# Optimization experiments

Measured on AMD Instinct MI355X. Metric: run time of the kernel, lower is better.

## Reference

```python
import jax, jax.numpy as jnp
import numpy as np

B, T, F, U, M = 4096, 16, 256, 512, 8
DELTA_T = 0.04

# ln_tau_table: tau = 1, 10^0.5, 10^1.0, ... -> ln(tau) = i * 0.5*ln(10)
LN_TAU = (jnp.arange(M, dtype=jnp.float32) * (0.5 * np.log(10.0))).astype(jnp.float32)
DECAY = jnp.exp(-DELTA_T / (LN_TAU + 1e-7))  # [M]


def setup_inputs() -> dict:
    key = jax.random.key(0)
    ks = jax.random.split(key, 9)
    s = lambda fan_in: 1.0 / np.sqrt(fan_in)
    return {
        "x": jax.random.normal(ks[0], (B, T, F), dtype=jnp.float32),
        "W_r": jax.random.normal(ks[1], (F + U, U * M), dtype=jnp.float32) * s(F + U),
        "b_r": jax.random.normal(ks[2], (U * M,), dtype=jnp.float32) * 0.01,
        "W_q": jax.random.normal(ks[3], (F + U, U), dtype=jnp.float32) * s(F + U),
        "b_q": jax.random.normal(ks[4], (U,), dtype=jnp.float32) * 0.01,
        "W_s": jax.random.normal(ks[5], (F + U, U * M), dtype=jnp.float32) * s(F + U),
        "b_s": jax.random.normal(ks[6], (U * M,), dtype=jnp.float32) * 0.01,
        "W_out": jax.random.normal(ks[7], (U, 3), dtype=jnp.float32) * s(U),
        "b_out": jax.random.normal(ks[8], (3,), dtype=jnp.float32) * 0.01,
    }


def _ctgru_forward(x, W_r, b_r, W_q, b_q, W_s, b_s, W_out, b_out):
    def step(h_hat, x_t):  # h_hat: [B,U,M], x_t: [B,F]
        h = h_hat.sum(axis=2)                              # [B,U]
        fused = jnp.concatenate([x_t, h], axis=1)          # [B,F+U]
        ln_tau_r = (fused @ W_r + b_r).reshape(-1, U, M)   # [B,U,M]
        r_ki = jax.nn.softmax(-jnp.square(ln_tau_r - LN_TAU), axis=2)
        q_in = jnp.concatenate([x_t, jnp.sum(r_ki * h_hat, axis=2)], axis=1)
        q_k = jnp.tanh(q_in @ W_q + b_q)[:, :, None]       # [B,U,1]
        ln_tau_s = (fused @ W_s + b_s).reshape(-1, U, M)
        s_ki = jax.nn.softmax(-jnp.square(ln_tau_s - LN_TAU), axis=2)
        h_next = ((1.0 - s_ki) * h_hat + s_ki * q_k) * DECAY
        return h_next, h_next.sum(axis=2)                  # carry, hidden [B,U]

    h0 = jnp.zeros((x.shape[0], U, M), dtype=x.dtype)
    _, hiddens = jax.lax.scan(step, h0, jnp.swapaxes(x, 0, 1))  # hiddens: [T,B,U]
    outputs = jnp.swapaxes(hiddens, 0, 1)                  # [B,T,U]
    return outputs @ W_out + b_out                         # [B,T,3]


def reference(x, W_r, b_r, W_q, b_q, W_s, b_s, W_out, b_out):
    return _ctgru_forward(x, W_r, b_r, W_q, b_q, W_s, b_s, W_out, b_out)
```

## Files before the change

kernel.cpp:

```cpp
#include <hip/hip_runtime.h>
#include <hip/hip_bf16.h>
#include <math.h>

#define B_   4096
#define T_   16
#define F_   256
#define U_   512
#define M_   8
#define K_   768
#define NRS  4096
#define NC   8192
#define LNT  1.1512925f

typedef __bf16 bf16_t;
typedef bf16_t bf16x8 __attribute__((ext_vector_type(8)));
typedef bf16_t bf16x4 __attribute__((ext_vector_type(4)));
typedef float  f32x4  __attribute__((ext_vector_type(4)));

__device__ inline void gl_lds16(const void* g, void* lds) {
    __builtin_amdgcn_global_load_lds(
        (const __attribute__((address_space(1))) unsigned int*)g,
        (__attribute__((address_space(3))) unsigned int*)lds, 16, 0, 0);
}

#define VMCNT(n) asm volatile("s_waitcnt vmcnt(" #n ")" ::: "memory")
#define LGKM0()  asm volatile("s_waitcnt lgkmcnt(0)" ::: "memory")
#define BAR()    __builtin_amdgcn_s_barrier()

__device__ inline void stageA(bf16_t* dst, const bf16_t* xt, const bf16_t* hp,
                              int m0, int k0, int tid) {
    const int r = tid >> 2;
    const int c = ((tid & 3) ^ ((tid >> 3) & 3)) * 8;
    const bf16_t *s0, *s1;
    if (k0 < F_) {
        s0 = xt + (size_t)(m0 + r) * F_ + k0 + c;
        s1 = xt + (size_t)(m0 + r + 128) * F_ + k0 + c;
    } else {
        s0 = hp + (size_t)(m0 + r) * U_ + (k0 - F_) + c;
        s1 = hp + (size_t)(m0 + r + 128) * U_ + (k0 - F_) + c;
    }
    gl_lds16(s0, (char*)dst + tid * 16);
    gl_lds16(s1, (char*)dst + (tid + 512) * 16);
}

__device__ inline void stageB(bf16_t* dst, const bf16_t* Bt, int n0, int k0, int tid) {
    const int r = tid >> 2;
    const int c = ((tid & 3) ^ ((tid >> 3) & 3)) * 8;
    gl_lds16(Bt + (size_t)(n0 + r) * K_ + k0 + c,       (char*)dst + tid * 16);
    gl_lds16(Bt + (size_t)(n0 + r + 128) * K_ + k0 + c, (char*)dst + (tid + 512) * 16);
}

__device__ inline void ds_read4(const bf16_t* base, bf16x8 (&v)[4]) {
    v[0] = *(const bf16x8*)(base);
    v[1] = *(const bf16x8*)(base + 512);
    v[2] = *(const bf16x8*)(base + 1024);
    v[3] = *(const bf16x8*)(base + 1536);
}

template <int H>
__device__ inline void mfma16(f32x4 (&acc)[8][4], const bf16x8 (&a)[4],
                              const bf16x8 (&b)[4]) {
    __builtin_amdgcn_s_setprio(1);
#pragma unroll
    for (int i = 0; i < 4; ++i)
#pragma unroll
        for (int j = 0; j < 4; ++j)
            acc[H * 4 + i][j] = __builtin_amdgcn_mfma_f32_16x16x32_bf16(
                a[i], b[j], acc[H * 4 + i][j], 0, 0, 0);
    __builtin_amdgcn_s_setprio(0);
}

__global__ __launch_bounds__(512, 2) void gemm_rs_p2(
    const bf16_t* __restrict__ xt,
    const bf16_t* __restrict__ hprev,
    const bf16_t* __restrict__ Bt,
    const float*  __restrict__ biasP,
    const bf16_t* __restrict__ hhat,
    bf16_t* __restrict__ rh,
    bf16_t* __restrict__ sbuf)
{
    __shared__ bf16_t Asl[2][256 * 32];
    __shared__ bf16_t Bsl[2][256 * 32];

    const int tid  = threadIdx.x;
    const int lane = tid & 63;
    const int wave = tid >> 6;

    const int lin = blockIdx.y * 16 + blockIdx.x;
    const int xcd = lin & 7, q = lin >> 3;
    const int m0 = ((xcd >> 1) * 4 + (q & 3)) * 256;
    const int n0 = ((xcd & 1) * 16 + (q >> 2)) * 256;

    const int wm = wave >> 2;
    const int wn = wave & 3;
    const int lr = lane & 15;
    const int kq = lane >> 4;
    const int cr = (kq ^ ((lr >> 1) & 3)) * 8;

    const int aoff0 = (wm * 128 + lr) * 32 + cr;
    const int aoff1 = (wm * 128 + 64 + lr) * 32 + cr;
    const int boff  = (wn * 64 + lr) * 32 + cr;

    f32x4 acc[8][4] = {};
    bf16x8 a[4], b[4];

    stageA(&Asl[0][0], xt, hprev, m0, 0, tid);
    stageB(&Bsl[0][0], Bt, n0, 0, tid);
    VMCNT(0);
    BAR();

#define TILE(T, SFLAG)                                                        \
  {                                                                           \
    const int p_ = (T) & 1, pn_ = p_ ^ 1;                                     \
    if (SFLAG) {                                                              \
      stageA(&Asl[pn_][0], xt, hprev, m0, ((T) + 1) * 32, tid);               \
      stageB(&Bsl[pn_][0], Bt, n0, ((T) + 1) * 32, tid);                      \
    }                                                                         \
    ds_read4(&Asl[p_][0] + aoff0, a);                                         \
    ds_read4(&Bsl[p_][0] + boff, b);                                          \
    LGKM0();                                                                  \
    mfma16<0>(acc, a, b);                                                     \
    ds_read4(&Asl[p_][0] + aoff1, a);                                         \
    LGKM0();                                                                  \
    mfma16<1>(acc, a, b);                                                     \
    VMCNT(0);                                                                 \
    BAR();                                                                    \
  }

    for (int tt = 0; tt < 22; tt += 2) { TILE(tt, 1); TILE(tt + 1, 1); }
    TILE(22, 1);
    TILE(23, 0);
#undef TILE

    const int nb  = n0 + wn * 64;
    const int u3  = lane & 7;
    const int m0v = ((lane >> 3) & 1) * 4;
    const bool is_r = nb < NRS;

    float bj[4];
#pragma unroll
    for (int j = 0; j < 4; ++j) bj[j] = biasP[nb + j * 16 + lr];

#pragma unroll
    for (int mi = 0; mi < 8; ++mi) {
        const int rowb = m0 + wm * 128 + mi * 16 + kq * 4;
#pragma unroll
        for (int r = 0; r < 4; ++r) {
            const int row = rowb + r;
            float e[4], sum = 0.f;
#pragma unroll
            for (int j = 0; j < 4; ++j) {
                float v = acc[mi][j][r] + bj[j];
                float d = v - (float)(m0v + j) * LNT;
                e[j] = __expf(-d * d);
                sum += e[j];
            }
            sum += __shfl_xor(sum, 8, 64);
            const float inv = 1.0f / sum;
            if (is_r) {
                bf16x4 h4 = *(const bf16x4*)(hhat + (size_t)row * NRS + nb + u3 * 8 + m0v);
                float rhv = 0.f;
#pragma unroll
                for (int j = 0; j < 4; ++j) rhv += e[j] * inv * (float)h4[j];
                rhv += __shfl_xor(rhv, 8, 64);
                if ((lane & 8) == 0)
                    rh[(size_t)row * U_ + (nb >> 3) + u3] = (bf16_t)rhv;
            } else {
                bf16x4 pv;
#pragma unroll
                for (int j = 0; j < 4; ++j) pv[j] = (bf16_t)(e[j] * inv);
                *(bf16x4*)(sbuf + (size_t)row * NRS + (nb - NRS) + u3 * 8 + m0v) = pv;
            }
        }
    }
}

__global__ __launch_bounds__(256) void gemm_q_up(
    const bf16_t* __restrict__ xt,
    const bf16_t* __restrict__ rh,
    const bf16_t* __restrict__ Bq,
    const float*  __restrict__ bq,
    const bf16_t* __restrict__ sbuf,
    bf16_t* __restrict__ hhat,
    bf16_t* __restrict__ hnext)
{
    __shared__ bf16_t Al[2][64 * 32];
    __shared__ bf16_t Bl[2][64 * 32];

    const int tid  = threadIdx.x;
    const int lane = tid & 63;
    const int wave = tid >> 6;
    const int m0 = blockIdx.x * 64;
    const int n0 = blockIdx.y * 64;
    const int wm = (wave & 1) * 32;
    const int wn = (wave >> 1) * 32;
    const int lr = lane & 15;
    const int kq = lane >> 4;

    f32x4 acc[2][2] = {};

    const int rA = tid >> 2;
    const int kc = (tid & 3) * 8;

    for (int kk = 0; kk < K_; kk += 64) {
        const bf16_t* arow;
        int cbase;
        if (kk < F_) { arow = xt + (size_t)(m0 + rA) * F_; cbase = kk; }
        else         { arow = rh + (size_t)(m0 + rA) * U_; cbase = kk - F_; }

        __syncthreads();
        gl_lds16(arow + cbase + kc,      (char*)&Al[0][0] + tid * 16);
        gl_lds16(arow + cbase + 32 + kc, (char*)&Al[1][0] + tid * 16);
        gl_lds16(Bq + (size_t)(n0 + rA) * K_ + kk + kc,      (char*)&Bl[0][0] + tid * 16);
        gl_lds16(Bq + (size_t)(n0 + rA) * K_ + kk + 32 + kc, (char*)&Bl[1][0] + tid * 16);
        __syncthreads();

#pragma unroll
        for (int s = 0; s < 2; s++) {
            bf16x8 af[2], bfr[2];
#pragma unroll
            for (int i = 0; i < 2; i++)
                af[i] = *(const bf16x8*)(&Al[s][0] + (wm + i * 16 + lr) * 32 + kq * 8);
#pragma unroll
            for (int i = 0; i < 2; i++)
                bfr[i] = *(const bf16x8*)(&Bl[s][0] + (wn + i * 16 + lr) * 32 + kq * 8);
#pragma unroll
            for (int i = 0; i < 2; i++)
#pragma unroll
                for (int j = 0; j < 2; j++)
                    acc[i][j] = __builtin_amdgcn_mfma_f32_16x16x32_bf16(
                        af[i], bfr[j], acc[i][j], 0, 0, 0);
        }
    }

    const float DEC[8] = {0.0f, 0.9658531f, 0.9827783f, 0.9884856f,
                          0.9913518f, 0.9930754f, 0.9942261f, 0.9950489f};

#pragma unroll
    for (int i = 0; i < 2; i++) {
        const int rowb = m0 + wm + i * 16 + kq * 4;
#pragma unroll
        for (int j = 0; j < 2; j++) {
            const int u = n0 + wn + j * 16 + lr;
            const float bv = bq[u];
#pragma unroll
            for (int r = 0; r < 4; r++) {
                const int row = rowb + r;
                const float q = tanhf(acc[i][j][r] + bv);
                const size_t base = (size_t)row * NRS + u * 8;
                bf16x8 s8 = *(const bf16x8*)(sbuf + base);
                bf16x8 h8 = *(const bf16x8*)(hhat + base);
                bf16x8 ho;
                float hs = 0.f;
#pragma unroll
                for (int m = 0; m < 8; m++) {
                    float s = (float)s8[m];
                    float h = (float)h8[m];
                    float hn = ((1.f - s) * h + s * q) * DEC[m];
                    ho[m] = (bf16_t)hn;
                    hs += hn;
                }
                *(bf16x8*)(hhat + base) = ho;
                hnext[(size_t)row * U_ + u] = (bf16_t)hs;
            }
        }
    }
}

__global__ void transpose_perm(const float* __restrict__ src, bf16_t* __restrict__ dst) {
    __shared__ float tl[32][33];
    int k0 = blockIdx.x * 32, n0 = blockIdx.y * 32;
    int tx = threadIdx.x & 31, ty = threadIdx.x >> 5;
#pragma unroll
    for (int i = 0; i < 32; i += 8)
        tl[ty + i][tx] = src[(size_t)(k0 + ty + i) * NRS + n0 + tx];
    __syncthreads();
#pragma unroll
    for (int i = 0; i < 32; i += 8) {
        int n = n0 + ty + i;
        int m = n & 7, u3v = (n >> 3) & 7;
        int p = (n & ~63) + (m & 3) * 16 + (m >> 2) * 8 + u3v;
        dst[(size_t)p * K_ + k0 + tx] = (bf16_t)tl[tx][ty + i];
    }
}

__global__ void transpose_plain(const float* __restrict__ src, bf16_t* __restrict__ dst, int N) {
    __shared__ float tl[32][33];
    int k0 = blockIdx.x * 32, n0 = blockIdx.y * 32;
    int tx = threadIdx.x & 31, ty = threadIdx.x >> 5;
#pragma unroll
    for (int i = 0; i < 32; i += 8)
        tl[ty + i][tx] = src[(size_t)(k0 + ty + i) * N + n0 + tx];
    __syncthreads();
#pragma unroll
    for (int i = 0; i < 32; i += 8)
        dst[(size_t)(n0 + ty + i) * K_ + k0 + tx] = (bf16_t)tl[tx][ty + i];
}

__global__ void bias_perm(const float* __restrict__ b_r, const float* __restrict__ b_s,
                          float* __restrict__ biasP) {
    int p = blockIdx.x * 256 + threadIdx.x;
    int pr = p & 63, j = pr >> 4, lr = pr & 15;
    int L = (p & ~63) + (lr & 7) * 8 + ((lr >> 3) & 1) * 4 + j;
    biasP[p] = (L < NRS) ? b_r[L] : b_s[L - NRS];
}

__global__ void xall_build(const float* __restrict__ x, bf16_t* __restrict__ xall) {
    int idx = blockIdx.x * 256 + threadIdx.x;
    int b = idx >> 12;
    int rem = idx & 4095;
    int t = rem >> 8, f = rem & 255;
    xall[((size_t)t * B_ + b) * F_ + f] = (bf16_t)x[idx];
}

__global__ __launch_bounds__(256) void out_all(
    const bf16_t* __restrict__ hall,
    const float* __restrict__ Wout,
    const float* __restrict__ bout,
    float* __restrict__ out)
{
    int row = blockIdx.x * 4 + (threadIdx.x >> 6);
    int lane = threadIdx.x & 63;
    bf16x8 h8 = *(const bf16x8*)(hall + (size_t)row * U_ + lane * 8);
    float p0 = 0, p1 = 0, p2 = 0;
#pragma unroll
    for (int k = 0; k < 8; k++) {
        float h = (float)h8[k];
        int u = lane * 8 + k;
        p0 += h * Wout[u * 3 + 0];
        p1 += h * Wout[u * 3 + 1];
        p2 += h * Wout[u * 3 + 2];
    }
    for (int off = 32; off; off >>= 1) {
        p0 += __shfl_down(p0, off, 64);
        p1 += __shfl_down(p1, off, 64);
        p2 += __shfl_down(p2, off, 64);
    }
    if (lane == 0) {
        int t = row >> 12, b = row & (B_ - 1);
        size_t o = ((size_t)b * T_ + t) * 3;
        out[o + 0] = p0 + bout[0];
        out[o + 1] = p1 + bout[1];
        out[o + 2] = p2 + bout[2];
    }
}

extern "C" void kernel_launch(void* const* d_in, const int* in_sizes, int n_in,
                              void* d_out, int out_size, void* d_ws, size_t ws_size,
                              hipStream_t stream) {
    const float* x   = (const float*)d_in[0];
    const float* W_r = (const float*)d_in[1];
    const float* b_r = (const float*)d_in[2];
    const float* W_q = (const float*)d_in[3];
    const float* b_q = (const float*)d_in[4];
    const float* W_s = (const float*)d_in[5];
    const float* b_s = (const float*)d_in[6];
    const float* W_o = (const float*)d_in[7];
    const float* b_o = (const float*)d_in[8];
    float* out = (float*)d_out;

    char* ws = (char*)d_ws;
    bf16_t* hhat  = (bf16_t*)ws; ws += (size_t)B_ * NRS * 2;
    bf16_t* sbuf  = (bf16_t*)ws; ws += (size_t)B_ * NRS * 2;
    bf16_t* xall  = (bf16_t*)ws; ws += (size_t)B_ * T_ * F_ * 2;
    bf16_t* hall  = (bf16_t*)ws; ws += (size_t)(T_ + 1) * B_ * U_ * 2;
    bf16_t* rh    = (bf16_t*)ws; ws += (size_t)B_ * U_ * 2;
    bf16_t* WrsT  = (bf16_t*)ws; ws += (size_t)NC * K_ * 2;
    bf16_t* WqT   = (bf16_t*)ws; ws += (size_t)U_ * K_ * 2;
    float*  biasP = (float*)ws;  ws += (size_t)NC * 4;

    hipMemsetAsync(hhat, 0, (size_t)B_ * NRS * 2, stream);
    hipMemsetAsync(hall, 0, (size_t)B_ * U_ * 2, stream);
    xall_build<<<B_ * T_ * F_ / 256, 256, 0, stream>>>(x, xall);
    transpose_perm<<<dim3(K_ / 32, NRS / 32), 256, 0, stream>>>(W_r, WrsT);
    transpose_perm<<<dim3(K_ / 32, NRS / 32), 256, 0, stream>>>(W_s, WrsT + (size_t)NRS * K_);
    transpose_plain<<<dim3(K_ / 32, U_ / 32), 256, 0, stream>>>(W_q, WqT, U_);
    bias_perm<<<NC / 256, 256, 0, stream>>>(b_r, b_s, biasP);

    for (int t = 0; t < T_; t++) {
        const bf16_t* xt = xall + (size_t)t * B_ * F_;
        const bf16_t* hp = hall + (size_t)t * B_ * U_;
        bf16_t*       hn = hall + (size_t)(t + 1) * B_ * U_;
        gemm_rs_p2<<<dim3(16, 32), 512, 0, stream>>>(xt, hp, WrsT, biasP, hhat, rh, sbuf);
        gemm_q_up<<<dim3(64, 8), 256, 0, stream>>>(xt, rh, WqT, b_q, sbuf, hhat, hn);
    }
    out_all<<<B_ * T_ / 4, 256, 0, stream>>>(hall + (size_t)B_ * U_, W_o, b_o, out);
}
```

Measured before the change: 1.803 ms.

## Pre-tile GEMM operands into contiguous swizzled 256x32 slots

The x inputs, the r/s weight matrix and the recurrent hidden state are stored in a blocked layout. Each 256-row by 32-column k-slice becomes one contiguous 16KB slot, with the LDS bank swizzle already applied. Staging into LDS in the main GEMM then becomes two fully contiguous global-to-LDS copies per thread, replacing strided row gathers with per-thread swizzle address math. The cost is a one-time weight re-tiling kernel, extra workspace, and scattered 2-byte writes of the hidden state into the tiled buffer in the q/update kernel on every step.

```diff
diff --git a/kernel.cpp b/kernel.cpp
--- a/kernel.cpp
+++ b/kernel.cpp
@@ -27,27 +27,9 @@
 #define LGKM0()  asm volatile("s_waitcnt lgkmcnt(0)" ::: "memory")
 #define BAR()    __builtin_amdgcn_s_barrier()
 
-__device__ inline void stageA(bf16_t* dst, const bf16_t* xt, const bf16_t* hp,
-                              int m0, int k0, int tid) {
-    const int r = tid >> 2;
-    const int c = ((tid & 3) ^ ((tid >> 3) & 3)) * 8;
-    const bf16_t *s0, *s1;
-    if (k0 < F_) {
-        s0 = xt + (size_t)(m0 + r) * F_ + k0 + c;
-        s1 = xt + (size_t)(m0 + r + 128) * F_ + k0 + c;
-    } else {
-        s0 = hp + (size_t)(m0 + r) * U_ + (k0 - F_) + c;
-        s1 = hp + (size_t)(m0 + r + 128) * U_ + (k0 - F_) + c;
-    }
-    gl_lds16(s0, (char*)dst + tid * 16);
-    gl_lds16(s1, (char*)dst + (tid + 512) * 16);
-}
-
-__device__ inline void stageB(bf16_t* dst, const bf16_t* Bt, int n0, int k0, int tid) {
-    const int r = tid >> 2;
-    const int c = ((tid & 3) ^ ((tid >> 3) & 3)) * 8;
-    gl_lds16(Bt + (size_t)(n0 + r) * K_ + k0 + c,       (char*)dst + tid * 16);
-    gl_lds16(Bt + (size_t)(n0 + r + 128) * K_ + k0 + c, (char*)dst + (tid + 512) * 16);
+__device__ inline void stage_slot(const bf16_t* src, bf16_t* dst, int tid) {
+    gl_lds16(src + tid * 8,        (char*)dst + tid * 16);
+    gl_lds16(src + tid * 8 + 4096, (char*)dst + tid * 16 + 8192);
 }
 
 __device__ inline void ds_read4(const bf16_t* base, bf16x8 (&v)[4]) {
@@ -70,17 +52,17 @@
     __builtin_amdgcn_s_setprio(0);
 }
 
-__global__ __launch_bounds__(512, 2) void gemm_rs_p2(
-    const bf16_t* __restrict__ xt,
-    const bf16_t* __restrict__ hprev,
+__global__ __launch_bounds__(512, 2) void gemm_rs_tp(
+    const bf16_t* __restrict__ xt_t,
+    const bf16_t* __restrict__ ht,
     const bf16_t* __restrict__ Bt,
     const float*  __restrict__ biasP,
     const bf16_t* __restrict__ hhat,
     bf16_t* __restrict__ rh,
     bf16_t* __restrict__ sbuf)
 {
-    __shared__ bf16_t Asl[2][256 * 32];
-    __shared__ bf16_t Bsl[2][256 * 32];
+    __shared__ __attribute__((aligned(16))) bf16_t Asl[2][8192];
+    __shared__ __attribute__((aligned(16))) bf16_t Bsl[2][8192];
 
     const int tid  = threadIdx.x;
     const int lane = tid & 63;
@@ -90,6 +72,7 @@
     const int xcd = lin & 7, q = lin >> 3;
     const int m0 = ((xcd >> 1) * 4 + (q & 3)) * 256;
     const int n0 = ((xcd & 1) * 16 + (q >> 2)) * 256;
+    const int mp = m0 >> 8, np = n0 >> 8;
 
     const int wm = wave >> 2;
     const int wn = wave & 3;
@@ -104,8 +87,12 @@
     f32x4 acc[8][4] = {};
     bf16x8 a[4], b[4];
 
-    stageA(&Asl[0][0], xt, hprev, m0, 0, tid);
-    stageB(&Bsl[0][0], Bt, n0, 0, tid);
+#define ASRC(S) ((S) < 8 ? xt_t + (size_t)(mp * 8 + (S)) * 8192               \
+                         : ht   + (size_t)(mp * 16 + (S) - 8) * 8192)
+#define BSRC(S) (Bt + (size_t)(np * 24 + (S)) * 8192)
+
+    stage_slot(ASRC(0), &Asl[0][0], tid);
+    stage_slot(BSRC(0), &Bsl[0][0], tid);
     VMCNT(0);
     BAR();
 
@@ -113,8 +100,8 @@
   {                                                                           \
     const int p_ = (T) & 1, pn_ = p_ ^ 1;                                     \
     if (SFLAG) {                                                              \
-      stageA(&Asl[pn_][0], xt, hprev, m0, ((T) + 1) * 32, tid);               \
-      stageB(&Bsl[pn_][0], Bt, n0, ((T) + 1) * 32, tid);                      \
+      stage_slot(ASRC((T) + 1), &Asl[pn_][0], tid);                           \
+      stage_slot(BSRC((T) + 1), &Bsl[pn_][0], tid);                           \
     }                                                                         \
     ds_read4(&Asl[p_][0] + aoff0, a);                                         \
     ds_read4(&Bsl[p_][0] + boff, b);                                          \
@@ -131,6 +118,8 @@
     TILE(22, 1);
     TILE(23, 0);
 #undef TILE
+#undef ASRC
+#undef BSRC
 
     const int nb  = n0 + wn * 64;
     const int u3  = lane & 7;
@@ -176,16 +165,17 @@
 }
 
 __global__ __launch_bounds__(256) void gemm_q_up(
-    const bf16_t* __restrict__ xt,
+    const bf16_t* __restrict__ xt_t,
     const bf16_t* __restrict__ rh,
     const bf16_t* __restrict__ Bq,
     const float*  __restrict__ bq,
     const bf16_t* __restrict__ sbuf,
     bf16_t* __restrict__ hhat,
-    bf16_t* __restrict__ hnext)
+    bf16_t* __restrict__ hnext,
+    bf16_t* __restrict__ htile)
 {
-    __shared__ bf16_t Al[2][64 * 32];
-    __shared__ bf16_t Bl[2][64 * 32];
+    __shared__ __attribute__((aligned(16))) bf16_t Al[2][64 * 32];
+    __shared__ __attribute__((aligned(16))) bf16_t Bl[2][64 * 32];
 
     const int tid  = threadIdx.x;
     const int lane = tid & 63;
@@ -196,21 +186,26 @@
     const int wn = (wave >> 1) * 32;
     const int lr = lane & 15;
     const int kq = lane >> 4;
+    const int crq = (kq ^ ((lr >> 1) & 3)) * 8;
 
     f32x4 acc[2][2] = {};
 
-    const int rA = tid >> 2;
-    const int kc = (tid & 3) * 8;
+    const int rA  = tid >> 2;
+    const int kc  = (tid & 3) * 8;
+    const int kcs = ((tid & 3) ^ ((tid >> 3) & 3)) * 8;
 
     for (int kk = 0; kk < K_; kk += 64) {
-        const bf16_t* arow;
-        int cbase;
-        if (kk < F_) { arow = xt + (size_t)(m0 + rA) * F_; cbase = kk; }
-        else         { arow = rh + (size_t)(m0 + rA) * U_; cbase = kk - F_; }
-
         __syncthreads();
-        gl_lds16(arow + cbase + kc,      (char*)&Al[0][0] + tid * 16);
-        gl_lds16(arow + cbase + 32 + kc, (char*)&Al[1][0] + tid * 16);
+        if (kk < F_) {
+            const bf16_t* s0p = xt_t + (size_t)((m0 >> 8) * 8 + (kk >> 5)) * 8192
+                                     + (size_t)(m0 & 255) * 32;
+            gl_lds16(s0p + tid * 8,        (char*)&Al[0][0] + tid * 16);
+            gl_lds16(s0p + 8192 + tid * 8, (char*)&Al[1][0] + tid * 16);
+        } else {
+            const int cb = kk - F_;
+            gl_lds16(rh + (size_t)(m0 + rA) * U_ + cb + kcs,      (char*)&Al[0][0] + tid * 16);
+            gl_lds16(rh + (size_t)(m0 + rA) * U_ + cb + 32 + kcs, (char*)&Al[1][0] + tid * 16);
+        }
         gl_lds16(Bq + (size_t)(n0 + rA) * K_ + kk + kc,      (char*)&Bl[0][0] + tid * 16);
         gl_lds16(Bq + (size_t)(n0 + rA) * K_ + kk + 32 + kc, (char*)&Bl[1][0] + tid * 16);
         __syncthreads();
@@ -220,7 +215,7 @@
             bf16x8 af[2], bfr[2];
 #pragma unroll
             for (int i = 0; i < 2; i++)
-                af[i] = *(const bf16x8*)(&Al[s][0] + (wm + i * 16 + lr) * 32 + kq * 8);
+                af[i] = *(const bf16x8*)(&Al[s][0] + (wm + i * 16 + lr) * 32 + crq);
 #pragma unroll
             for (int i = 0; i < 2; i++)
                 bfr[i] = *(const bf16x8*)(&Bl[s][0] + (wn + i * 16 + lr) * 32 + kq * 8);
@@ -243,6 +238,7 @@
         for (int j = 0; j < 2; j++) {
             const int u = n0 + wn + j * 16 + lr;
             const float bv = bq[u];
+            const int us = u >> 5, uc = u & 31;
 #pragma unroll
             for (int r = 0; r < 4; r++) {
                 const int row = rowb + r;
@@ -262,6 +258,9 @@
                 }
                 *(bf16x8*)(hhat + base) = ho;
                 hnext[(size_t)row * U_ + u] = (bf16_t)hs;
+                const int rl = row & 255;
+                htile[(size_t)((row >> 8) * 16 + us) * 8192 + rl * 32
+                      + (((uc >> 3) ^ ((rl >> 1) & 3)) * 8) + (uc & 7)] = (bf16_t)hs;
             }
         }
     }
@@ -282,6 +281,14 @@
         int p = (n & ~63) + (m & 3) * 16 + (m >> 2) * 8 + u3v;
         dst[(size_t)p * K_ + k0 + tx] = (bf16_t)tl[tx][ty + i];
     }
+}
+
+__global__ void btile_build(const bf16_t* __restrict__ WrsT, bf16_t* __restrict__ Bt) {
+    int n = blockIdx.x / 3;
+    int k = (blockIdx.x % 3) * 256 + threadIdx.x;
+    int p = n >> 8, r = n & 255, s = k >> 5, c = k & 31;
+    Bt[(size_t)(p * 24 + s) * 8192 + r * 32
+       + (((c >> 3) ^ ((r >> 1) & 3)) * 8) + (c & 7)] = WrsT[(size_t)n * K_ + k];
 }
 
 __global__ void transpose_plain(const float* __restrict__ src, bf16_t* __restrict__ dst, int N) {
@@ -305,12 +312,14 @@
     biasP[p] = (L < NRS) ? b_r[L] : b_s[L - NRS];
 }
 
-__global__ void xall_build(const float* __restrict__ x, bf16_t* __restrict__ xall) {
+__global__ void xtile_build(const float* __restrict__ x, bf16_t* __restrict__ xt) {
     int idx = blockIdx.x * 256 + threadIdx.x;
     int b = idx >> 12;
     int rem = idx & 4095;
     int t = rem >> 8, f = rem & 255;
-    xall[((size_t)t * B_ + b) * F_ + f] = (bf16_t)x[idx];
+    int mp = b >> 8, r = b & 255, s = f >> 5, c = f & 31;
+    xt[((size_t)(t * 16 + mp) * 8 + s) * 8192 + r * 32
+       + (((c >> 3) ^ ((r >> 1) & 3)) * 8) + (c & 7)] = (bf16_t)x[idx];
 }
 
 __global__ __launch_bounds__(256) void out_all(
@@ -362,27 +371,29 @@
     char* ws = (char*)d_ws;
     bf16_t* hhat  = (bf16_t*)ws; ws += (size_t)B_ * NRS * 2;
     bf16_t* sbuf  = (bf16_t*)ws; ws += (size_t)B_ * NRS * 2;
-    bf16_t* xall  = (bf16_t*)ws; ws += (size_t)B_ * T_ * F_ * 2;
+    bf16_t* xtile = (bf16_t*)ws; ws += (size_t)B_ * T_ * F_ * 2;
     bf16_t* hall  = (bf16_t*)ws; ws += (size_t)(T_ + 1) * B_ * U_ * 2;
     bf16_t* rh    = (bf16_t*)ws; ws += (size_t)B_ * U_ * 2;
     bf16_t* WrsT  = (bf16_t*)ws; ws += (size_t)NC * K_ * 2;
+    bf16_t* Btile = (bf16_t*)ws; ws += (size_t)NC * K_ * 2;
+    bf16_t* htile = (bf16_t*)ws; ws += (size_t)B_ * U_ * 2;
     bf16_t* WqT   = (bf16_t*)ws; ws += (size_t)U_ * K_ * 2;
     float*  biasP = (float*)ws;  ws += (size_t)NC * 4;
 
     hipMemsetAsync(hhat, 0, (size_t)B_ * NRS * 2, stream);
-    hipMemsetAsync(hall, 0, (size_t)B_ * U_ * 2, stream);
-    xall_build<<<B_ * T_ * F_ / 256, 256, 0, stream>>>(x, xall);
+    hipMemsetAsync(htile, 0, (size_t)B_ * U_ * 2, stream);
+    xtile_build<<<B_ * T_ * F_ / 256, 256, 0, stream>>>(x, xtile);
     transpose_perm<<<dim3(K_ / 32, NRS / 32), 256, 0, stream>>>(W_r, WrsT);
     transpose_perm<<<dim3(K_ / 32, NRS / 32), 256, 0, stream>>>(W_s, WrsT + (size_t)NRS * K_);
+    btile_build<<<NC * 3, 256, 0, stream>>>(WrsT, Btile);
     transpose_plain<<<dim3(K_ / 32, U_ / 32), 256, 0, stream>>>(W_q, WqT, U_);
     bias_perm<<<NC / 256, 256, 0, stream>>>(b_r, b_s, biasP);
 
     for (int t = 0; t < T_; t++) {
-        const bf16_t* xt = xall + (size_t)t * B_ * F_;
-        const bf16_t* hp = hall + (size_t)t * B_ * U_;
-        bf16_t*       hn = hall + (size_t)(t + 1) * B_ * U_;
-        gemm_rs_p2<<<dim3(16, 32), 512, 0, stream>>>(xt, hp, WrsT, biasP, hhat, rh, sbuf);
-        gemm_q_up<<<dim3(64, 8), 256, 0, stream>>>(xt, rh, WqT, b_q, sbuf, hhat, hn);
+        const bf16_t* xt_t = xtile + (size_t)t * 16 * 8 * 8192;
+        bf16_t*       hn   = hall + (size_t)(t + 1) * B_ * U_;
+        gemm_rs_tp<<<dim3(16, 32), 512, 0, stream>>>(xt_t, htile, Btile, biasP, hhat, rh, sbuf);
+        gemm_q_up<<<dim3(64, 8), 256, 0, stream>>>(xt_t, rh, WqT, b_q, sbuf, hhat, hn, htile);
     }
     out_all<<<B_ * T_ / 4, 256, 0, stream>>>(hall + (size_t)B_ * U_, W_o, b_o, out);
 }
```

After: 1.792 ms. Within noise of the previous version (-0.6%).
